# Kernel optimization log

Measured on AMD Instinct MI355X. Metric: run time of the kernel, lower is better.

## Reference

```python
import jax, jax.numpy as jnp
import numpy as np

U, I, K = 100000, 50000, 64
N_II_LAYERS = 2
N_UI_LAYERS = 3
EPS = 1e-12  # torch F.normalize default eps


def spmm(src, dst, w, x, n):
    # out[dst] += w * x[src]  (COO sparse-dense matmul, LGConv with normalize=False)
    return jax.ops.segment_sum(x[src] * w[:, None], dst, num_segments=n)


def l2norm(x):
    # torch.nn.functional.normalize(x, p=2, dim=1)
    return x / jnp.maximum(jnp.linalg.norm(x, axis=1, keepdims=True), EPS)


def setup_inputs() -> dict:
    key = jax.random.key(0)
    ks = jax.random.split(key, 9)
    E_II, E_UI = 1600000, 4800000
    return {
        "Gu": jax.random.normal(ks[0], (U, K), dtype=jnp.float32),
        "Gi": jax.random.normal(ks[1], (I, K), dtype=jnp.float32),
        "Gis": jax.random.normal(ks[2], (I, K), dtype=jnp.float32),
        "ii_w": jax.random.uniform(ks[3], (E_II,), dtype=jnp.float32),
        "ui_w": jax.random.uniform(ks[4], (E_UI,), dtype=jnp.float32),
        "ii_src": jax.random.randint(ks[5], (E_II,), 0, I, dtype=jnp.int32),
        "ii_dst": jax.random.randint(ks[6], (E_II,), 0, I, dtype=jnp.int32),
        "ui_src": jax.random.randint(ks[7], (E_UI,), 0, U + I, dtype=jnp.int32),
        "ui_dst": jax.random.randint(ks[8], (E_UI,), 0, U + I, dtype=jnp.int32),
    }


def reference(Gu, Gi, Gis, ii_w, ui_w, ii_src, ii_dst, ui_src, ui_dst):
    # item-item propagation (n_ii_layers LGConv, no per-layer norm)
    gis = Gis
    for _ in range(N_II_LAYERS):
        gis = spmm(ii_src, ii_dst, ii_w, gis, I)
    # user-item propagation with per-layer L2 normalize
    ego = jnp.concatenate([Gu, Gi], axis=0)  # [U+I, K]
    all_emb = [ego]
    for layer in range(N_UI_LAYERS):
        all_emb.append(l2norm(spmm(ui_src, ui_dst, ui_w, all_emb[layer], U + I)))
    mean_emb = jnp.mean(jnp.stack(all_emb, axis=1), axis=1)  # [U+I, K]
    gu, gi = mean_emb[:U], mean_emb[U:]
    return gu, gi + l2norm(gis)
```

## Files before the change

### kernel.cpp

```cpp
#include <hip/hip_runtime.h>
#include <hip/hip_bf16.h>

constexpr int U_N = 100000;
constexpr int I_N = 50000;
constexpr int KDIM = 64;
constexpr float EPSF = 1e-12f;

constexpr int RPB = 256;
constexpr int BSHIFT = 8;
constexpr int CH = 4096;

typedef float f4 __attribute__((ext_vector_type(4)));
typedef unsigned short u16;

__device__ inline f4 ld4(const float* p) { return *(const f4*)p; }

__device__ inline unsigned pack_bf16(float a, float b) {
    unsigned ua = __float_as_uint(a);
    unsigned ub = __float_as_uint(b);
    ua += 0x7fffu + ((ua >> 16) & 1u);
    ub += 0x7fffu + ((ub >> 16) & 1u);
    return (ua >> 16) | (ub & 0xffff0000u);
}

__device__ inline void bf8_to_f32(uint4 u, float* f) {
    unsigned w0 = u.x, w1 = u.y, w2 = u.z, w3 = u.w;
    f[0] = __uint_as_float(w0 << 16);  f[1] = __uint_as_float(w0 & 0xffff0000u);
    f[2] = __uint_as_float(w1 << 16);  f[3] = __uint_as_float(w1 & 0xffff0000u);
    f[4] = __uint_as_float(w2 << 16);  f[5] = __uint_as_float(w2 & 0xffff0000u);
    f[6] = __uint_as_float(w3 << 16);  f[7] = __uint_as_float(w3 & 0xffff0000u);
}

__global__ void bhist2_k(const int* __restrict__ dstU, int* __restrict__ cntU, int EU, int NBu,
                         const int* __restrict__ dstI, int* __restrict__ cntI, int EI, int NBi,
                         int GU, int GTOT) {
    const int* dst; int* cnt; int E; int NB; int nbk; int bid;
    if ((int)blockIdx.x < GU) { dst = dstU; cnt = cntU; E = EU; NB = NBu; nbk = GU; bid = blockIdx.x; }
    else { dst = dstI; cnt = cntI; E = EI; NB = NBi; nbk = GTOT - GU; bid = blockIdx.x - GU; }
    __shared__ int h[1024];
    int t = threadIdx.x;
    for (int i = t; i < 1024; i += 256) h[i] = 0;
    __syncthreads();
    int stride = nbk * 256 * 4;
    for (int i = (bid * 256 + t) * 4; i < E; i += stride) {
        if (i + 4 <= E) {
            int4 d = *(const int4*)(dst + i);
            atomicAdd(&h[d.x >> BSHIFT], 1);
            atomicAdd(&h[d.y >> BSHIFT], 1);
            atomicAdd(&h[d.z >> BSHIFT], 1);
            atomicAdd(&h[d.w >> BSHIFT], 1);
        } else {
            for (int k = i; k < E; ++k) atomicAdd(&h[dst[k] >> BSHIFT], 1);
        }
    }
    __syncthreads();
    for (int i = t; i < NB; i += 256) if (h[i]) atomicAdd(&cnt[i], h[i]);
}

__global__ void bscan2_k(const int* __restrict__ cntU, int* __restrict__ baseU,
                         int* __restrict__ curU, int NBu,
                         const int* __restrict__ cntI, int* __restrict__ baseI,
                         int* __restrict__ curI, int NBi) {
    __shared__ int s[1024];
    int t = threadIdx.x;
    int c = (t < NBu) ? cntU[t] : 0;
    s[t] = c;
    __syncthreads();
    for (int off = 1; off < 1024; off <<= 1) {
        int v = s[t] + ((t >= off) ? s[t - off] : 0);
        __syncthreads();
        s[t] = v;
        __syncthreads();
    }
    if (t < NBu) { baseU[t] = s[t] - c; curU[t] = s[t] - c; }
    if (t == NBu - 1) baseU[NBu] = s[t];
    __syncthreads();
    int c2 = (t < NBi) ? cntI[t] : 0;
    s[t] = c2;
    __syncthreads();
    for (int off = 1; off < 1024; off <<= 1) {
        int v = s[t] + ((t >= off) ? s[t - off] : 0);
        __syncthreads();
        s[t] = v;
        __syncthreads();
    }
    if (t < NBi) { baseI[t] = s[t] - c2; curI[t] = s[t] - c2; }
    if (t == NBi - 1) baseI[NBi] = s[t];
}

__global__ __launch_bounds__(1024) void bpart2_k(
        const int* __restrict__ srcU, const int* __restrict__ dstU,
        const float* __restrict__ wU, int* __restrict__ curU,
        int2* __restrict__ pairsU, int nchU, int EU,
        const int* __restrict__ srcI, const int* __restrict__ dstI,
        const float* __restrict__ wI, int* __restrict__ curI,
        int2* __restrict__ pairsI, int nchI, int EI) {
    __shared__ int hist[1024];
    __shared__ int sA[1024];
    __shared__ int rb[1024];
    __shared__ int2 stp[CH];
    __shared__ unsigned stg[CH];
    int t = threadIdx.x;
    int ntot = nchU + nchI;
    for (int c = blockIdx.x; c < ntot; c += gridDim.x) {
        const int* src; const int* dst; const float* w; int* gcur; int2* pairs;
        int cb, E;
        if (c < nchU) { src = srcU; dst = dstU; w = wU; gcur = curU; pairs = pairsU;
                        cb = c * CH; E = EU; }
        else          { src = srcI; dst = dstI; w = wI; gcur = curI; pairs = pairsI;
                        cb = (c - nchU) * CH; E = EI; }
        int n = min(CH, E - cb);
        hist[t] = 0;
        __syncthreads();
        int esrc[4], ew[4], ebkt[4];
        bool ev[4];
#pragma unroll
        for (int k = 0; k < 4; ++k) {
            int j = k * 1024 + t;
            ev[k] = j < n;
            if (ev[k]) {
                int i = cb + j;
                int d = dst[i];
                esrc[k] = src[i];
                ew[k] = (int)((__float_as_uint(w[i]) & 0xFFFFFF00u) | (unsigned)(d & (RPB - 1)));
                ebkt[k] = d >> BSHIFT;
                atomicAdd(&hist[ebkt[k]], 1);
            }
        }
        __syncthreads();
        int cnt_t = hist[t];
        sA[t] = cnt_t;
        __syncthreads();
        for (int off = 1; off < 1024; off <<= 1) {
            int v = sA[t] + ((t >= off) ? sA[t - off] : 0);
            __syncthreads();
            sA[t] = v;
            __syncthreads();
        }
        sA[t] -= cnt_t;
        if (cnt_t > 0) rb[t] = atomicAdd(&gcur[t], cnt_t);
        hist[t] = 0;
        __syncthreads();
#pragma unroll
        for (int k = 0; k < 4; ++k) {
            if (ev[k]) {
                int b = ebkt[k];
                int local = atomicAdd(&hist[b], 1);
                int pos = sA[b] + local;
                stp[pos] = make_int2(esrc[k], ew[k]);
                stg[pos] = (unsigned)(rb[b] + local);
            }
        }
        __syncthreads();
#pragma unroll
        for (int k = 0; k < 4; ++k) {
            int p = k * 1024 + t;
            if (p < n) pairs[stg[p]] = stp[p];
        }
        __syncthreads();
    }
}

__global__ __launch_bounds__(1024) void bfill2_k(
        const int* __restrict__ baseU, const int2* __restrict__ pairsU,
        int2* __restrict__ e2U, int* __restrict__ startU, int NBu, int NRu,
        const int* __restrict__ baseI, const int2* __restrict__ pairsI,
        int2* __restrict__ e2I, int* __restrict__ startI, int NBi, int NRi) {
    __shared__ int hist[RPB];
    __shared__ int pos[RPB + 1];
    int t = threadIdx.x;
    int ntot = NBu + NBi;
    for (int b = blockIdx.x; b < ntot; b += gridDim.x) {
        const int* base; const int2* pairs; int2* e2; int* start; int bb, Nrows;
        if (b < NBu) { base = baseU; pairs = pairsU; e2 = e2U; start = startU;
                       bb = b; Nrows = NRu; }
        else         { base = baseI; pairs = pairsI; e2 = e2I; start = startI;
                       bb = b - NBu; Nrows = NRi; }
        int gb = base[bb];
        int cnt = base[bb + 1] - gb;
        if (t < RPB) hist[t] = 0;
        __syncthreads();
        for (int i = t; i < cnt; i += 1024) atomicAdd(&hist[pairs[gb + i].y & (RPB - 1)], 1);
        __syncthreads();
        if (t < RPB) pos[t] = hist[t];
        __syncthreads();
        for (int off = 1; off < RPB; off <<= 1) {
            int v = 0;
            if (t < RPB) v = pos[t] + ((t >= off) ? pos[t - off] : 0);
            __syncthreads();
            if (t < RPB) pos[t] = v;
            __syncthreads();
        }
        int myv = 0;
        if (t < RPB) myv = (t == 0) ? 0 : pos[t - 1];
        __syncthreads();
        if (t < RPB) pos[t] = myv;
        if (t == 0) pos[RPB] = cnt;
        __syncthreads();
        int r0 = bb * RPB;
        if (t <= RPB) {
            int row = r0 + t;
            if (row <= Nrows) start[row] = gb + pos[t];
        }
        __syncthreads();
        for (int i = t; i < cnt; i += 1024) {
            int2 pe = pairs[gb + i];
            int r = pe.y & (RPB - 1);
            int p = atomicAdd(&pos[r], 1);
            e2[gb + p] = make_int2(pe.x, pe.y & ~(RPB - 1));
        }
        __syncthreads();
    }
}


__device__ inline float group8_sum(float v) {
    v += __shfl_xor(v, 1, 64);
    v += __shfl_xor(v, 2, 64);
    v += __shfl_xor(v, 4, 64);
    return v;
}

__device__ inline void spmm_row_bf(const int2* __restrict__ e2, int j0, int j1,
                                   const u16* __restrict__ x, int g, int l,
                                   float a[8]) {
    float a0[8] = {0, 0, 0, 0, 0, 0, 0, 0};
    float a1[8] = {0, 0, 0, 0, 0, 0, 0, 0};
    int j = j0;
    for (; j + 16 <= j1; j += 16) {
        int2 ea = e2[j + g];
        int2 eb = e2[j + 8 + g];
        uint4 ua = *(const uint4*)(x + (size_t)ea.x * KDIM + l * 8);
        uint4 ub = *(const uint4*)(x + (size_t)eb.x * KDIM + l * 8);
        float wa = __int_as_float(ea.y), wb = __int_as_float(eb.y);
        float fa[8], fb[8];
        bf8_to_f32(ua, fa);
        bf8_to_f32(ub, fb);
#pragma unroll
        for (int c = 0; c < 8; ++c) {
            a0[c] += wa * fa[c];
            a1[c] += wb * fb[c];
        }
    }
    for (; j < j1; j += 8) {
        if (j + g < j1) {
            int2 ea = e2[j + g];
            uint4 ua = *(const uint4*)(x + (size_t)ea.x * KDIM + l * 8);
            float wa = __int_as_float(ea.y);
            float fa[8];
            bf8_to_f32(ua, fa);
#pragma unroll
            for (int c = 0; c < 8; ++c) a0[c] += wa * fa[c];
        }
    }
#pragma unroll
    for (int c = 0; c < 8; ++c) {
        float v = a0[c] + a1[c];
        v += __shfl_xor(v, 8, 64);
        v += __shfl_xor(v, 16, 64);
        v += __shfl_xor(v, 32, 64);
        a[c] = v;
    }
}

__global__ void cvt_all(const float* __restrict__ Gu, const float* __restrict__ Gi,
                        const float* __restrict__ Gis, u16* __restrict__ bufA,
                        u16* __restrict__ gis0, int nu8, int na8, int ntot8) {
    int i = blockIdx.x * blockDim.x + threadIdx.x;
    if (i >= ntot8) return;
    const float* p;
    u16* o;
    if (i < nu8)      { p = Gu  + (size_t)i * 8;          o = bufA + (size_t)i * 8; }
    else if (i < na8) { p = Gi  + (size_t)(i - nu8) * 8;  o = bufA + (size_t)i * 8; }
    else              { p = Gis + (size_t)(i - na8) * 8;  o = gis0 + (size_t)(i - na8) * 8; }
    f4 v0 = ld4(p);
    f4 v1 = ld4(p + 4);
    uint4 pk;
    pk.x = pack_bf16(v0.x, v0.y);
    pk.y = pack_bf16(v0.z, v0.w);
    pk.z = pack_bf16(v1.x, v1.y);
    pk.w = pack_bf16(v1.z, v1.w);
    *(uint4*)o = pk;
}

__global__ void spmm_pull_bf(const int* __restrict__ start, const int2* __restrict__ e2,
                             const u16* __restrict__ x, u16* __restrict__ y, int nrows) {
    const int lane = threadIdx.x & 63;
    const int g = lane >> 3, l = lane & 7;
    const int r = (blockIdx.x * blockDim.x + threadIdx.x) >> 6;
    if (r >= nrows) return;
    float a[8];
    spmm_row_bf(e2, start[r], start[r + 1], x, g, l, a);
    if (g == 0) {
        uint4 pk;
        pk.x = pack_bf16(a[0], a[1]);
        pk.y = pack_bf16(a[2], a[3]);
        pk.z = pack_bf16(a[4], a[5]);
        pk.w = pack_bf16(a[6], a[7]);
        *(uint4*)(y + (size_t)r * KDIM + l * 8) = pk;
    }
}

__global__ void spmm_pull_f32(const int* __restrict__ start, const int2* __restrict__ e2,
                              const u16* __restrict__ x, float* __restrict__ y, int nrows) {
    const int lane = threadIdx.x & 63;
    const int g = lane >> 3, l = lane & 7;
    const int r = (blockIdx.x * blockDim.x + threadIdx.x) >> 6;
    if (r >= nrows) return;
    float a[8];
    spmm_row_bf(e2, start[r], start[r + 1], x, g, l, a);
    if (g == 0) {
        float* yp = y + (size_t)r * KDIM + l * 8;
        *(f4*)yp = f4{a[0], a[1], a[2], a[3]};
        *(f4*)(yp + 4) = f4{a[4], a[5], a[6], a[7]};
    }
}

__global__ void spmm_pull_norm_noacc(const int* __restrict__ start, const int2* __restrict__ e2,
                                     const u16* __restrict__ x, u16* __restrict__ cur,
                                     int nrows) {
    const int lane = threadIdx.x & 63;
    const int g = lane >> 3, l = lane & 7;
    const int r = (blockIdx.x * blockDim.x + threadIdx.x) >> 6;
    if (r >= nrows) return;
    float a[8];
    spmm_row_bf(e2, start[r], start[r + 1], x, g, l, a);
    float loc = 0.f;
#pragma unroll
    for (int c = 0; c < 8; ++c) loc += a[c] * a[c];
    float ss = group8_sum(loc);
    float inv = 1.f / fmaxf(sqrtf(ss), EPSF);
    if (g == 0) {
        uint4 pk;
        pk.x = pack_bf16(a[0] * inv, a[1] * inv);
        pk.y = pack_bf16(a[2] * inv, a[3] * inv);
        pk.z = pack_bf16(a[4] * inv, a[5] * inv);
        pk.w = pack_bf16(a[6] * inv, a[7] * inv);
        *(uint4*)(cur + (size_t)r * KDIM + l * 8) = pk;
    }
}

__global__ void spmm_pull_norm_final(const int* __restrict__ start, const int2* __restrict__ e2,
                                     const u16* __restrict__ x,
                                     const u16* __restrict__ n1,
                                     const float* __restrict__ Gu,
                                     const float* __restrict__ Gi,
                                     const float* __restrict__ gis,
                                     float* __restrict__ out, int nrows) {
    const int lane = threadIdx.x & 63;
    const int g = lane >> 3, l = lane & 7;
    const int r = (blockIdx.x * blockDim.x + threadIdx.x) >> 6;
    if (r >= nrows) return;
    float a[8];
    spmm_row_bf(e2, start[r], start[r + 1], x, g, l, a);
    float loc = 0.f;
#pragma unroll
    for (int c = 0; c < 8; ++c) loc += a[c] * a[c];
    float ss = group8_sum(loc);
    float inv = 1.f / fmaxf(sqrtf(ss), EPSF);
    if (g != 0) return;
    const float* ep = (r < U_N) ? Gu + (size_t)r * KDIM + l * 8
                                : Gi + (size_t)(r - U_N) * KDIM + l * 8;
    f4 e0 = __builtin_nontemporal_load((const f4*)ep);
    f4 e1 = __builtin_nontemporal_load((const f4*)(ep + 4));
    uint4 u1 = *(const uint4*)(n1 + (size_t)r * KDIM + l * 8);
    uint4 u2 = *(const uint4*)(x + (size_t)r * KDIM + l * 8);
    float f1[8], f2[8];
    bf8_to_f32(u1, f1);
    bf8_to_f32(u2, f2);
    f4 v0 = (e0 + f4{f1[0], f1[1], f1[2], f1[3]} + f4{f2[0], f2[1], f2[2], f2[3]}
                + f4{a[0] * inv, a[1] * inv, a[2] * inv, a[3] * inv}) * 0.25f;
    f4 v1 = (e1 + f4{f1[4], f1[5], f1[6], f1[7]} + f4{f2[4], f2[5], f2[6], f2[7]}
                + f4{a[4] * inv, a[5] * inv, a[6] * inv, a[7] * inv}) * 0.25f;
    if (r >= U_N) {
        const float* gp = gis + (size_t)(r - U_N) * KDIM + l * 8;
        f4 g0 = ld4(gp);
        f4 g1 = ld4(gp + 4);
        float loc2 = g0.x * g0.x + g0.y * g0.y + g0.z * g0.z + g0.w * g0.w
                   + g1.x * g1.x + g1.y * g1.y + g1.z * g1.z + g1.w * g1.w;
        float ss2 = group8_sum(loc2);
        float inv2 = 1.f / fmaxf(sqrtf(ss2), EPSF);
        v0 += g0 * inv2;
        v1 += g1 * inv2;
    }
    float* op = out + (size_t)r * KDIM + l * 8;
    __builtin_nontemporal_store(v0, (f4*)op);
    __builtin_nontemporal_store(v1, (f4*)(op + 4));
}

extern "C" void kernel_launch(void* const* d_in, const int* in_sizes, int n_in,
                              void* d_out, int out_size, void* d_ws, size_t ws_size,
                              hipStream_t stream) {
    const float* Gu     = (const float*)d_in[0];
    const float* Gi     = (const float*)d_in[1];
    const float* Gis    = (const float*)d_in[2];
    const float* ii_w   = (const float*)d_in[3];
    const float* ui_w   = (const float*)d_in[4];
    const int*   ii_src = (const int*)d_in[5];
    const int*   ii_dst = (const int*)d_in[6];
    const int*   ui_src = (const int*)d_in[7];
    const int*   ui_dst = (const int*)d_in[8];
    const int E_II = in_sizes[5];
    const int E_UI = in_sizes[7];

    const int NR    = U_N + I_N;
    const size_t NI = (size_t)I_N * KDIM;
    const size_t NA = (size_t)NR * KDIM;

    u16*  bufA = (u16*)d_ws;
    u16*  bufB = bufA + NA;
    u16*  gis0 = bufB + NA;
    u16*  gisA = gis0 + NI;
    float* gisB = (float*)(gisA + NI);
    int2*  ui_e = (int2*)(gisB + NI);
    int2*  ii_e = ui_e + E_UI;
    int*   ui_start = (int*)(ii_e + E_II);
    int*   ii_start = ui_start + (NR + 1);
    int*   bkt_cnt  = ii_start + (I_N + 1);
    int*   bkt_base = bkt_cnt + 1024;
    int*   bkt_cur  = bkt_base + 1056;

    int2* pairsU = (int2*)bufA;
    int2* pairsI = (int2*)gis0;

    float* out = (float*)d_out;

    const int NB_UI = (NR + RPB - 1) / RPB;
    const int NB_II = (I_N + RPB - 1) / RPB;
    int* cntU  = bkt_cnt;
    int* cntI  = bkt_cnt + NB_UI;
    int* baseU = bkt_base;
    int* baseI = bkt_base + (NB_UI + 1);
    int* curU  = bkt_cur;
    int* curI  = bkt_cur + NB_UI;

    const int nchU = (E_UI + CH - 1) / CH;
    const int nchI = (E_II + CH - 1) / CH;

    hipMemsetAsync(bkt_cnt, 0, (NB_UI + NB_II) * sizeof(int), stream);
    bhist2_k<<<1024, 256, 0, stream>>>(ui_dst, cntU, E_UI, NB_UI,
                                       ii_dst, cntI, E_II, NB_II, 768, 1024);
    bscan2_k<<<1, 1024, 0, stream>>>(cntU, baseU, curU, NB_UI,
                                     cntI, baseI, curI, NB_II);
    bpart2_k<<<512, 1024, 0, stream>>>(ui_src, ui_dst, ui_w, curU, pairsU, nchU, E_UI,
                                       ii_src, ii_dst, ii_w, curI, pairsI, nchI, E_II);
    bfill2_k<<<512, 1024, 0, stream>>>(baseU, pairsU, ui_e, ui_start, NB_UI, NR,
                                       baseI, pairsI, ii_e, ii_start, NB_II, I_N);

    const int nu8 = (int)((size_t)U_N * KDIM / 8);
    const int na8 = (int)(NA / 8);
    const int nt8 = (int)((NA + NI) / 8);
    cvt_all<<<(nt8 + 255) / 256, 256, 0, stream>>>(Gu, Gi, Gis, bufA, gis0, nu8, na8, nt8);

    spmm_pull_bf<<<(I_N + 3) / 4, 256, 0, stream>>>(ii_start, ii_e, gis0, gisA, I_N);
    spmm_pull_f32<<<(I_N + 3) / 4, 256, 0, stream>>>(ii_start, ii_e, gisA, gisB, I_N);

    spmm_pull_norm_noacc<<<(NR + 3) / 4, 256, 0, stream>>>(ui_start, ui_e, bufA, bufB, NR);
    spmm_pull_norm_noacc<<<(NR + 3) / 4, 256, 0, stream>>>(ui_start, ui_e, bufB, bufA, NR);
    spmm_pull_norm_final<<<(NR + 3) / 4, 256, 0, stream>>>(ui_start, ui_e, bufA, bufB,
                                                           Gu, Gi, gisB, out, NR);
}
```

Baseline: 622.4 us.

## Fuse item-item and user-item SpMM layers, stage bucket pairs in LDS

Merges the two item-item SpMM launches with the first two user-item layers into two combined launches, so the independent propagations share a grid and fewer kernels run back to back. Replaces the barrier-heavy shared-memory Hillis-Steele scan in the partition kernel with a wavefront-shuffle scan. Stages each bucket's pairs in LDS in the fill kernel so global pairs are read once instead of twice. The large LDS staging buffer (96KB) may reduce occupancy of the fill kernel.

```diff
diff --git a/kernel.cpp b/kernel.cpp
--- a/kernel.cpp
+++ b/kernel.cpp
@@ -9,6 +9,7 @@
 constexpr int RPB = 256;
 constexpr int BSHIFT = 8;
 constexpr int CH = 4096;
+constexpr int CAP = 12288;
 
 typedef float f4 __attribute__((ext_vector_type(4)));
 typedef unsigned short u16;
@@ -98,6 +99,7 @@
     __shared__ int hist[1024];
     __shared__ int sA[1024];
     __shared__ int rb[1024];
+    __shared__ int wsum[16];
     __shared__ int2 stp[CH];
     __shared__ unsigned stg[CH];
     int t = threadIdx.x;
@@ -129,16 +131,27 @@
         }
         __syncthreads();
         int cnt_t = hist[t];
-        sA[t] = cnt_t;
-        __syncthreads();
-        for (int off = 1; off < 1024; off <<= 1) {
-            int v = sA[t] + ((t >= off) ? sA[t - off] : 0);
-            __syncthreads();
-            sA[t] = v;
-            __syncthreads();
-        }
-        sA[t] -= cnt_t;
-        if (cnt_t > 0) rb[t] = atomicAdd(&gcur[t], cnt_t);
+        int v = cnt_t;
+#pragma unroll
+        for (int off = 1; off < 64; off <<= 1) {
+            int nn = __shfl_up(v, off, 64);
+            if ((t & 63) >= off) v += nn;
+        }
+        if ((t & 63) == 63) wsum[t >> 6] = v;
+        __syncthreads();
+        if (t < 16) {
+            int x = wsum[t];
+#pragma unroll
+            for (int off = 1; off < 16; off <<= 1) {
+                int nn = __shfl_up(x, off, 16);
+                if (t >= off) x += nn;
+            }
+            wsum[t] = x;
+        }
+        __syncthreads();
+        int ex = v - cnt_t + ((t >= 64) ? wsum[(t >> 6) - 1] : 0);
+        sA[t] = ex;
+        rb[t] = (cnt_t > 0) ? atomicAdd(&gcur[t], cnt_t) : 0;
         hist[t] = 0;
         __syncthreads();
 #pragma unroll
@@ -166,6 +179,7 @@
         int2* __restrict__ e2U, int* __restrict__ startU, int NBu, int NRu,
         const int* __restrict__ baseI, const int2* __restrict__ pairsI,
         int2* __restrict__ e2I, int* __restrict__ startI, int NBi, int NRi) {
+    __shared__ int2 st[CAP];
     __shared__ int hist[RPB];
     __shared__ int pos[RPB + 1];
     int t = threadIdx.x;
@@ -178,9 +192,19 @@
                        bb = b - NBu; Nrows = NRi; }
         int gb = base[bb];
         int cnt = base[bb + 1] - gb;
+        bool staged = (cnt <= CAP);
         if (t < RPB) hist[t] = 0;
         __syncthreads();
-        for (int i = t; i < cnt; i += 1024) atomicAdd(&hist[pairs[gb + i].y & (RPB - 1)], 1);
+        if (staged) {
+            for (int i = t; i < cnt; i += 1024) {
+                int2 pe = pairs[gb + i];
+                st[i] = pe;
+                atomicAdd(&hist[pe.y & (RPB - 1)], 1);
+            }
+        } else {
+            for (int i = t; i < cnt; i += 1024)
+                atomicAdd(&hist[pairs[gb + i].y & (RPB - 1)], 1);
+        }
         __syncthreads();
         if (t < RPB) pos[t] = hist[t];
         __syncthreads();
@@ -203,11 +227,20 @@
             if (row <= Nrows) start[row] = gb + pos[t];
         }
         __syncthreads();
-        for (int i = t; i < cnt; i += 1024) {
-            int2 pe = pairs[gb + i];
-            int r = pe.y & (RPB - 1);
-            int p = atomicAdd(&pos[r], 1);
-            e2[gb + p] = make_int2(pe.x, pe.y & ~(RPB - 1));
+        if (staged) {
+            for (int i = t; i < cnt; i += 1024) {
+                int2 pe = st[i];
+                int r = pe.y & (RPB - 1);
+                int p = atomicAdd(&pos[r], 1);
+                e2[gb + p] = make_int2(pe.x, pe.y & ~(RPB - 1));
+            }
+        } else {
+            for (int i = t; i < cnt; i += 1024) {
+                int2 pe = pairs[gb + i];
+                int r = pe.y & (RPB - 1);
+                int p = atomicAdd(&pos[r], 1);
+                e2[gb + p] = make_int2(pe.x, pe.y & ~(RPB - 1));
+            }
         }
         __syncthreads();
     }
@@ -283,60 +316,78 @@
     *(uint4*)o = pk;
 }
 
-__global__ void spmm_pull_bf(const int* __restrict__ start, const int2* __restrict__ e2,
-                             const u16* __restrict__ x, u16* __restrict__ y, int nrows) {
+__global__ void spmm_fused_l1(const int* __restrict__ ui_start, const int2* __restrict__ ui_e,
+                              const u16* __restrict__ xu, u16* __restrict__ yu,
+                              const int* __restrict__ ii_start, const int2* __restrict__ ii_e,
+                              const u16* __restrict__ xi, u16* __restrict__ yi,
+                              int nui, int nii) {
     const int lane = threadIdx.x & 63;
     const int g = lane >> 3, l = lane & 7;
     const int r = (blockIdx.x * blockDim.x + threadIdx.x) >> 6;
-    if (r >= nrows) return;
-    float a[8];
-    spmm_row_bf(e2, start[r], start[r + 1], x, g, l, a);
-    if (g == 0) {
-        uint4 pk;
-        pk.x = pack_bf16(a[0], a[1]);
-        pk.y = pack_bf16(a[2], a[3]);
-        pk.z = pack_bf16(a[4], a[5]);
-        pk.w = pack_bf16(a[6], a[7]);
-        *(uint4*)(y + (size_t)r * KDIM + l * 8) = pk;
-    }
-}
-
-__global__ void spmm_pull_f32(const int* __restrict__ start, const int2* __restrict__ e2,
-                              const u16* __restrict__ x, float* __restrict__ y, int nrows) {
+    if (r < nui) {
+        float a[8];
+        spmm_row_bf(ui_e, ui_start[r], ui_start[r + 1], xu, g, l, a);
+        float loc = 0.f;
+#pragma unroll
+        for (int c = 0; c < 8; ++c) loc += a[c] * a[c];
+        float ss = group8_sum(loc);
+        float inv = 1.f / fmaxf(sqrtf(ss), EPSF);
+        if (g == 0) {
+            uint4 pk;
+            pk.x = pack_bf16(a[0] * inv, a[1] * inv);
+            pk.y = pack_bf16(a[2] * inv, a[3] * inv);
+            pk.z = pack_bf16(a[4] * inv, a[5] * inv);
+            pk.w = pack_bf16(a[6] * inv, a[7] * inv);
+            *(uint4*)(yu + (size_t)r * KDIM + l * 8) = pk;
+        }
+    } else if (r < nui + nii) {
+        int rr = r - nui;
+        float a[8];
+        spmm_row_bf(ii_e, ii_start[rr], ii_start[rr + 1], xi, g, l, a);
+        if (g == 0) {
+            uint4 pk;
+            pk.x = pack_bf16(a[0], a[1]);
+            pk.y = pack_bf16(a[2], a[3]);
+            pk.z = pack_bf16(a[4], a[5]);
+            pk.w = pack_bf16(a[6], a[7]);
+            *(uint4*)(yi + (size_t)rr * KDIM + l * 8) = pk;
+        }
+    }
+}
+
+__global__ void spmm_fused_l2(const int* __restrict__ ui_start, const int2* __restrict__ ui_e,
+                              const u16* __restrict__ xu, u16* __restrict__ yu,
+                              const int* __restrict__ ii_start, const int2* __restrict__ ii_e,
+                              const u16* __restrict__ xi, float* __restrict__ yi,
+                              int nui, int nii) {
     const int lane = threadIdx.x & 63;
     const int g = lane >> 3, l = lane & 7;
     const int r = (blockIdx.x * blockDim.x + threadIdx.x) >> 6;
-    if (r >= nrows) return;
-    float a[8];
-    spmm_row_bf(e2, start[r], start[r + 1], x, g, l, a);
-    if (g == 0) {
-        float* yp = y + (size_t)r * KDIM + l * 8;
-        *(f4*)yp = f4{a[0], a[1], a[2], a[3]};
-        *(f4*)(yp + 4) = f4{a[4], a[5], a[6], a[7]};
-    }
-}
-
-__global__ void spmm_pull_norm_noacc(const int* __restrict__ start, const int2* __restrict__ e2,
-                                     const u16* __restrict__ x, u16* __restrict__ cur,
-                                     int nrows) {
-    const int lane = threadIdx.x & 63;
-    const int g = lane >> 3, l = lane & 7;
-    const int r = (blockIdx.x * blockDim.x + threadIdx.x) >> 6;
-    if (r >= nrows) return;
-    float a[8];
-    spmm_row_bf(e2, start[r], start[r + 1], x, g, l, a);
-    float loc = 0.f;
-#pragma unroll
-    for (int c = 0; c < 8; ++c) loc += a[c] * a[c];
-    float ss = group8_sum(loc);
-    float inv = 1.f / fmaxf(sqrtf(ss), EPSF);
-    if (g == 0) {
-        uint4 pk;
-        pk.x = pack_bf16(a[0] * inv, a[1] * inv);
-        pk.y = pack_bf16(a[2] * inv, a[3] * inv);
-        pk.z = pack_bf16(a[4] * inv, a[5] * inv);
-        pk.w = pack_bf16(a[6] * inv, a[7] * inv);
-        *(uint4*)(cur + (size_t)r * KDIM + l * 8) = pk;
+    if (r < nui) {
+        float a[8];
+        spmm_row_bf(ui_e, ui_start[r], ui_start[r + 1], xu, g, l, a);
+        float loc = 0.f;
+#pragma unroll
+        for (int c = 0; c < 8; ++c) loc += a[c] * a[c];
+        float ss = group8_sum(loc);
+        float inv = 1.f / fmaxf(sqrtf(ss), EPSF);
+        if (g == 0) {
+            uint4 pk;
+            pk.x = pack_bf16(a[0] * inv, a[1] * inv);
+            pk.y = pack_bf16(a[2] * inv, a[3] * inv);
+            pk.z = pack_bf16(a[4] * inv, a[5] * inv);
+            pk.w = pack_bf16(a[6] * inv, a[7] * inv);
+            *(uint4*)(yu + (size_t)r * KDIM + l * 8) = pk;
+        }
+    } else if (r < nui + nii) {
+        int rr = r - nui;
+        float a[8];
+        spmm_row_bf(ii_e, ii_start[rr], ii_start[rr + 1], xi, g, l, a);
+        if (g == 0) {
+            float* yp = yi + (size_t)rr * KDIM + l * 8;
+            *(f4*)yp = f4{a[0], a[1], a[2], a[3]};
+            *(f4*)(yp + 4) = f4{a[4], a[5], a[6], a[7]};
+        }
     }
 }
 
@@ -452,11 +503,11 @@
     const int nt8 = (int)((NA + NI) / 8);
     cvt_all<<<(nt8 + 255) / 256, 256, 0, stream>>>(Gu, Gi, Gis, bufA, gis0, nu8, na8, nt8);
 
-    spmm_pull_bf<<<(I_N + 3) / 4, 256, 0, stream>>>(ii_start, ii_e, gis0, gisA, I_N);
-    spmm_pull_f32<<<(I_N + 3) / 4, 256, 0, stream>>>(ii_start, ii_e, gisA, gisB, I_N);
-
-    spmm_pull_norm_noacc<<<(NR + 3) / 4, 256, 0, stream>>>(ui_start, ui_e, bufA, bufB, NR);
-    spmm_pull_norm_noacc<<<(NR + 3) / 4, 256, 0, stream>>>(ui_start, ui_e, bufB, bufA, NR);
+    const int NTOT = NR + I_N;
+    spmm_fused_l1<<<(NTOT + 3) / 4, 256, 0, stream>>>(ui_start, ui_e, bufA, bufB,
+                                                      ii_start, ii_e, gis0, gisA, NR, I_N);
+    spmm_fused_l2<<<(NTOT + 3) / 4, 256, 0, stream>>>(ui_start, ui_e, bufB, bufA,
+                                                      ii_start, ii_e, gisA, gisB, NR, I_N);
     spmm_pull_norm_final<<<(NR + 3) / 4, 256, 0, stream>>>(ui_start, ui_e, bufA, bufB,
                                                            Gu, Gi, gisB, out, NR);
 }
```

Measured after the change: 607.3 us. -2.4%, faster.
